# Kernel tuning notes

Measured on AMD Instinct MI355X. Metric: run time of the kernel, lower is better.

## Reference

```python
import jax, jax.numpy as jnp
import numpy as np

B, C, H, W = 2, 256, 64, 64
FEAT = 256          # in_channels * expansion_ratio
HEADS = 8
HS = FEAT // HEADS  # 32
OUT = 256


def setup_inputs() -> dict:
    key = jax.random.key(0)
    ks = jax.random.split(key, 12)
    inp = {
        "x": jax.random.normal(ks[0], (B, C, H, W), jnp.float32),
        "mod_multiplier": jax.random.normal(ks[1], (B, FEAT), jnp.float32),
        "mod_bias": jax.random.normal(ks[2], (B, FEAT), jnp.float32),
        # learned parameters (1x1 convs as matrices)
        "w_qkv": jax.random.normal(ks[3], (3 * FEAT, C), jnp.float32) * 0.02,
        "b_qkv": jnp.zeros((3 * FEAT,), jnp.float32),
        "w_proj": jax.random.normal(ks[4], (OUT, FEAT), jnp.float32) * 0.02,
        "pe_q_h": jax.random.normal(ks[5], (1, FEAT, H, 1), jnp.float32) * 0.02,
        "pe_q_w": jax.random.normal(ks[6], (1, FEAT, 1, W), jnp.float32) * 0.02,
        "pe_k_h": jax.random.normal(ks[7], (1, FEAT, H, 1), jnp.float32) * 0.02,
        "pe_k_w": jax.random.normal(ks[8], (1, FEAT, 1, W), jnp.float32) * 0.02,
        "pre_act_bias": jnp.zeros((1, C, 1, 1), jnp.float32),
        "pre_qkv_bias": jnp.zeros((1, C, 1, 1), jnp.float32),
        "pre_proj_bias": jnp.zeros((1, FEAT, 1, 1), jnp.float32),
        "id_scale": jnp.ones((1, OUT, 1, 1), jnp.float32),
    }
    return inp


def reference(x, mod_multiplier, mod_bias, w_qkv, b_qkv, w_proj,
              pe_q_h, pe_q_w, pe_k_h, pe_k_w,
              pre_act_bias, pre_qkv_bias, pre_proj_bias, id_scale):
    b = x.shape[0]
    # pre-activation (Fixup-style biases)
    x_preact = jax.nn.silu(x + pre_act_bias) + pre_qkv_bias
    # 1x1 conv -> QKV: [b, 3F, H, W]
    qkv = jnp.einsum('bchw,oc->bohw', x_preact, w_qkv) + b_qkv[None, :, None, None]
    q, k, v = jnp.split(qkv, 3, axis=1)
    # additive positional embeddings
    q = q + pe_q_h + pe_q_w
    k = k + pe_k_h + pe_k_w
    # FiLM modulation of query
    q = q * mod_multiplier[:, :, None, None] + mod_bias[:, :, None, None]
    # [b, heads, head_size, H*W]
    q = q.reshape(b, HEADS, HS, H * W)
    k = k.reshape(b, HEADS, HS, H * W)
    v = v.reshape(b, HEADS, HS, H * W)
    scale = jnp.asarray(HS ** 0.5, x.dtype)
    logits = jnp.einsum('bhdn,bhdm->bhnm', q, k) / scale
    weights = jax.nn.softmax(logits, axis=-1)
    attn = jnp.einsum('bhnm,bhdm->bhdn', weights, v)
    attn = attn.reshape(b, FEAT, H, W)
    # output projection (1x1 conv, no bias)
    x_res = jnp.einsum('bchw,oc->bohw', attn + pre_proj_bias, w_proj)
    return x * id_scale + x_res
```

## Files before the change

### kernel.cpp

```cpp
#include <hip/hip_runtime.h>
#include <hip/hip_bf16.h>
#include <cstdint>

#define NB   2
#define NC   256
#define NN   4096
#define NH   8
#define HSZ  32
#define NF   256
#define N3F  768

typedef __bf16 bf16x8 __attribute__((ext_vector_type(8)));
typedef __bf16 bf16x4 __attribute__((ext_vector_type(4)));
typedef short  s16x4  __attribute__((ext_vector_type(4)));
typedef float  floatx4 __attribute__((ext_vector_type(4)));

#define QSCALE 0.25506601622184f

__global__ void k_prep(const float* __restrict__ x, const float* __restrict__ pab,
                       const float* __restrict__ pqb, __bf16* __restrict__ y,
                       const float* __restrict__ wqkv, const float* __restrict__ wproj,
                       __bf16* __restrict__ wqb, __bf16* __restrict__ wpb) {
    __shared__ __bf16 ct[32 * 264];
    int bid = blockIdx.x, tid = threadIdx.x;
    if (bid >= 256) {
        int id = (bid - 256) * 1024 + tid * 4;
        const float* src = (id < 196608) ? (wqkv + id) : (wproj + (id - 196608));
        __bf16* dst = (id < 196608) ? (wqb + id) : (wpb + (id - 196608));
        float4 v = *(const float4*)src;
        bf16x4 o;
        o[0] = (__bf16)v.x; o[1] = (__bf16)v.y; o[2] = (__bf16)v.z; o[3] = (__bf16)v.w;
        *(bf16x4*)dst = o;
        return;
    }
    int b = bid >> 7, nt = bid & 127;
    int n0 = nt * 32;
    int cbase = tid >> 3, nc = tid & 7;
#pragma unroll
    for (int q = 0; q < 8; q++) {
        int c = cbase + q * 32;
        const float4 xv = *(const float4*)(x + ((size_t)b * NC + c) * NN + n0 + nc * 4);
        float bias = pab[c], qb = pqb[c];
        float vs[4] = {xv.x, xv.y, xv.z, xv.w};
#pragma unroll
        for (int i = 0; i < 4; i++) {
            float s = vs[i] + bias;
            float r = s / (1.f + __expf(-s)) + qb;
            ct[(nc * 4 + i) * 264 + c] = (__bf16)r;
        }
    }
    __syncthreads();
#pragma unroll
    for (int q = 0; q < 4; q++) {
        int id = tid + q * 256;
        int n = id >> 5, ck = (id & 31) * 8;
        bf16x8 v = *(const bf16x8*)(ct + n * 264 + ck);
        *(bf16x8*)(y + ((size_t)b * NN + n0 + n) * NC + ck) = v;
    }
}

__launch_bounds__(256)
__global__ void k_qkv(const __bf16* __restrict__ y, const __bf16* __restrict__ wb,
                      const float* __restrict__ bqkv,
                      const float* __restrict__ peqh, const float* __restrict__ peqw,
                      const float* __restrict__ pekh, const float* __restrict__ pekw,
                      const float* __restrict__ mm, const float* __restrict__ mb,
                      __bf16* __restrict__ qs, __bf16* __restrict__ kf, __bf16* __restrict__ vf) {
    __shared__ __bf16 smem[4][64 * 40];
    __bf16* ct = &smem[0][0];
    const int nt = blockIdx.x, ot = blockIdx.y, b = blockIdx.z;
    const int tid = threadIdx.x;
    const int wave = tid >> 6, lane = tid & 63, ln = lane & 15, quad = lane >> 4;
    const int wm = (wave & 1) * 32, wn = (wave >> 1) * 32;
    floatx4 acc[2][2];
#pragma unroll
    for (int i = 0; i < 2; i++)
#pragma unroll
        for (int j = 0; j < 2; j++) acc[i][j] = 0.f;
    const __bf16* ysrc = y + ((size_t)b * NN + nt * 64) * NC;
    const __bf16* wsrc = wb + (size_t)ot * 64 * NC;
    const int r0 = tid >> 2, c0 = (tid & 3) * 8;
    bf16x8 ya = *(const bf16x8*)(ysrc + (size_t)r0 * NC + c0);
    bf16x8 wa = *(const bf16x8*)(wsrc + (size_t)r0 * NC + c0);
    for (int ko = 0; ko < 8; ko++) {
        int buf = ko & 1;
        *(bf16x8*)(&smem[buf][r0 * 40 + c0]) = ya;
        *(bf16x8*)(&smem[2 + buf][r0 * 40 + c0]) = wa;
        __syncthreads();
        if (ko < 7) {
            int kc = (ko + 1) * 32;
            ya = *(const bf16x8*)(ysrc + (size_t)r0 * NC + kc + c0);
            wa = *(const bf16x8*)(wsrc + (size_t)r0 * NC + kc + c0);
        }
        bf16x8 af[2], bfr[2];
#pragma unroll
        for (int ii = 0; ii < 2; ii++) af[ii]  = *(const bf16x8*)(&smem[buf][(wm + ii * 16 + ln) * 40 + quad * 8]);
#pragma unroll
        for (int jj = 0; jj < 2; jj++) bfr[jj] = *(const bf16x8*)(&smem[2 + buf][(wn + jj * 16 + ln) * 40 + quad * 8]);
#pragma unroll
        for (int ii = 0; ii < 2; ii++)
#pragma unroll
            for (int jj = 0; jj < 2; jj++)
                acc[ii][jj] = __builtin_amdgcn_mfma_f32_16x16x32_bf16(af[ii], bfr[jj], acc[ii][jj], 0, 0, 0);
    }
    __syncthreads();
    if (ot < 8) {
#pragma unroll
        for (int ii = 0; ii < 2; ii++)
#pragma unroll
            for (int jj = 0; jj < 2; jj++) {
                int o_l = wn + jj * 16 + ln;
                int o_g = ot * 64 + o_l;
                float bq = bqkv[o_g];
#pragma unroll
                for (int r = 0; r < 4; r++) {
                    int n_l = wm + ii * 16 + quad * 4 + r;
                    float val = acc[ii][jj][r] + bq;
                    if (ot < 4) {
                        val += peqh[o_g * 64 + nt] + peqw[o_g * 64 + n_l];
                        val = val * mm[b * NF + o_g] + mb[b * NF + o_g];
                        val *= QSCALE;
                    } else {
                        int c = o_g - 256;
                        val += pekh[c * 64 + nt] + pekw[c * 64 + n_l];
                    }
                    ct[n_l * 72 + o_l] = (__bf16)val;
                }
            }
        __syncthreads();
#pragma unroll
        for (int q = 0; q < 2; q++) {
            int id = tid + q * 256;
            int n_l = id >> 3, oc = (id & 7) * 8;
            bf16x8 v = *(const bf16x8*)(ct + n_l * 72 + oc);
            int n_g = nt * 64 + n_l;
            int o_g = ot * 64 + oc;
            if (ot < 4) {
                int h = o_g >> 5, d = o_g & 31;
                *(bf16x8*)(qs + (((size_t)b * NH + h) * NN + n_g) * HSZ + d) = v;
            } else {
                int c = o_g - 256, h = c >> 5, d0 = c & 31;
                size_t blk = ((size_t)(b * NH + h) * 256 + (n_g >> 4)) * 512;
                *(bf16x8*)(kf + blk + (d0 >> 3) * 128 + (n_g & 15) * 8) = v;
            }
        }
    } else {
#pragma unroll
        for (int ii = 0; ii < 2; ii++)
#pragma unroll
            for (int jj = 0; jj < 2; jj++) {
                int o_l = wn + jj * 16 + ln;
                float bq = bqkv[ot * 64 + o_l];
#pragma unroll
                for (int r = 0; r < 4; r++) {
                    int n_l = wm + ii * 16 + quad * 4 + r;
                    ct[o_l * 72 + n_l] = (__bf16)(acc[ii][jj][r] + bq);
                }
            }
        __syncthreads();
#pragma unroll
        for (int q = 0; q < 4; q++) {
            int id = tid + q * 256;
            int o_l = id >> 4, ng4 = (id & 15) * 4;
            bf16x4 v = *(const bf16x4*)(ct + o_l * 72 + ng4);
            int c = (ot - 8) * 64 + o_l, h = c >> 5, d = c & 31;
            int dj = d >> 4, lnv = d & 15;
            int m_g = nt * 64 + ng4;
            size_t blk = ((size_t)(b * NH + h) * 256 + (m_g >> 4)) * 512;
            *(bf16x4*)(vf + blk + (((m_g >> 2) & 3) * 16 + lnv) * 8 + dj * 4) = v;
        }
    }
}

__launch_bounds__(256)
__global__ void k_attn(const __bf16* __restrict__ qs, const __bf16* __restrict__ kf,
                       const __bf16* __restrict__ vf,
                       __bf16* __restrict__ po, float* __restrict__ pl) {
    __shared__ __bf16 sbuf[2 * 8192];
    int bi = blockIdx.x;
    int xcd = bi & 7, r = bi >> 3;
    int bh = xcd * 2 + (r & 1);
    int r2 = r >> 1;
    int qt = r2 & 31, half = r2 >> 5;
    int tid = threadIdx.x, wave = tid >> 6, lane = tid & 63, ln = lane & 15, quad = lane >> 4;
    int n0 = qt * 128 + wave * 32;
    const __bf16* qbase = qs + (size_t)bh * NN * HSZ;
    const __bf16* kfb = kf + ((size_t)bh * 256 + half * 128) * 512;
    const __bf16* vfb = vf + ((size_t)bh * 256 + half * 128) * 512;
    bf16x8 qa[2];
    qa[0] = *(const bf16x8*)(qbase + (size_t)(n0 + ln) * HSZ + quad * 8);
    qa[1] = *(const bf16x8*)(qbase + (size_t)(n0 + 16 + ln) * HSZ + quad * 8);
    floatx4 o[2][2], o2[2];
    o[0][0] = 0.f; o[0][1] = 0.f; o[1][0] = 0.f; o[1][1] = 0.f;
    o2[0] = 0.f; o2[1] = 0.f;
    floatx4 zf = 0.f;
    s16x4 ones;
    ones[0] = (short)0x3F80; ones[1] = (short)0x3F80;
    ones[2] = (short)0x3F80; ones[3] = (short)0x3F80;
    const int toff = tid * 8;
    const int lo = lane * 8;
    bf16x8 kr0, kr1, vr0, vr1;
    kr0 = *(const bf16x8*)(kfb + toff);
    kr1 = *(const bf16x8*)(kfb + toff + 2048);
    vr0 = *(const bf16x8*)(vfb + toff);
    vr1 = *(const bf16x8*)(vfb + toff + 2048);
    for (int mt = 0; mt < 16; mt++) {
        int bo = (mt & 1) << 13;
        *(bf16x8*)(sbuf + bo + toff) = kr0;
        *(bf16x8*)(sbuf + bo + toff + 2048) = kr1;
        *(bf16x8*)(sbuf + bo + 4096 + toff) = vr0;
        *(bf16x8*)(sbuf + bo + 4096 + toff + 2048) = vr1;
        __syncthreads();
        if (mt < 15) {
            const __bf16* kn = kfb + (mt + 1) * 4096;
            const __bf16* vn = vfb + (mt + 1) * 4096;
            kr0 = *(const bf16x8*)(kn + toff);
            kr1 = *(const bf16x8*)(kn + toff + 2048);
            vr0 = *(const bf16x8*)(vn + toff);
            vr1 = *(const bf16x8*)(vn + toff + 2048);
        }
        const __bf16* kl = sbuf + bo;
        const __bf16* vl = sbuf + bo + 4096;
#pragma unroll
        for (int j = 0; j < 8; j++) {
            bf16x8 kfr = *(const bf16x8*)(kl + j * 512 + lo);
            bf16x8 vfr = *(const bf16x8*)(vl + j * 512 + lo);
            s16x4 vb0, vb1;
            __builtin_memcpy(&vb0, &vfr, 8);
            __builtin_memcpy(&vb1, (const char*)&vfr + 8, 8);
#pragma unroll
            for (int i = 0; i < 2; i++) {
                floatx4 s = __builtin_amdgcn_mfma_f32_16x16x32_bf16(kfr, qa[i], zf, 0, 0, 0);
                bf16x4 p;
#pragma unroll
                for (int rr = 0; rr < 4; rr++)
                    p[rr] = (__bf16)__builtin_amdgcn_exp2f(s[rr]);
                s16x4 pa;
                __builtin_memcpy(&pa, &p, 8);
                o[i][0] = __builtin_amdgcn_mfma_f32_16x16x16bf16_1k(pa, vb0, o[i][0], 0, 0, 0);
                o[i][1] = __builtin_amdgcn_mfma_f32_16x16x16bf16_1k(pa, vb1, o[i][1], 0, 0, 0);
                o2[i]   = __builtin_amdgcn_mfma_f32_16x16x16bf16_1k(pa, ones, o2[i], 0, 0, 0);
            }
        }
    }
    size_t plbase = (size_t)(half * 16 + bh) * NN;
    if (ln == 0)
#pragma unroll
        for (int i = 0; i < 2; i++)
#pragma unroll
            for (int rr = 0; rr < 4; rr++)
                pl[plbase + n0 + i * 16 + quad * 4 + rr] = o2[i][rr];
    __bf16* ct = sbuf;
#pragma unroll
    for (int i = 0; i < 2; i++)
#pragma unroll
        for (int dj = 0; dj < 2; dj++)
#pragma unroll
            for (int rr = 0; rr < 4; rr++)
                ct[(wave * 32 + i * 16 + quad * 4 + rr) * 32 + dj * 16 + ln] = (__bf16)o[i][dj][rr];
    __syncthreads();
    size_t pobase = ((size_t)(half * 16 + bh) * NN + (size_t)qt * 128) * HSZ;
#pragma unroll
    for (int q = 0; q < 2; q++) {
        int id = tid + q * 256;
        int n_l = id >> 2, dc = (id & 3) * 8;
        *(bf16x8*)(po + pobase + n_l * HSZ + dc) = *(const bf16x8*)(ct + n_l * 32 + dc);
    }
}

__launch_bounds__(256)
__global__ void k_proj(const __bf16* __restrict__ po, const float* __restrict__ pl,
                       const __bf16* __restrict__ wpb, const float* __restrict__ ppb,
                       const float* __restrict__ x, const float* __restrict__ idsc,
                       float* __restrict__ out) {
    __shared__ __bf16 at[64 * 264];
    __shared__ __bf16 bt[2][64 * 40];
    __shared__ float linv[8 * 64];
    __shared__ float ppbs[256];
    int nt = blockIdx.x, ot = blockIdx.y, b = blockIdx.z;
    int tid = threadIdx.x, wave = tid >> 6, lane = tid & 63, ln = lane & 15, quad = lane >> 4;
    int wo = (wave & 1) * 32, wn = (wave >> 1) * 32;
#pragma unroll
    for (int q = 0; q < 8; q++) {
        int id = tid + q * 256;
        int row = id >> 5, fc = (id & 31) * 8;
        *(bf16x8*)(at + row * 264 + fc) = *(const bf16x8*)(wpb + (size_t)(ot * 64 + row) * NF + fc);
    }
#pragma unroll
    for (int q = 0; q < 2; q++) {
        int id = tid + q * 256;
        int h = id >> 6, n_l = id & 63;
        size_t base = (size_t)(b * NH + h) * NN + nt * 64 + n_l;
        linv[id] = 1.f / (pl[base] + pl[base + (size_t)16 * NN]);
    }
    ppbs[tid] = ppb[tid];
    __syncthreads();
    floatx4 acc[2][2];
#pragma unroll
    for (int i = 0; i < 2; i++)
#pragma unroll
        for (int j = 0; j < 2; j++) acc[i][j] = 0.f;
    const int n_l = tid >> 2, dh8 = (tid & 3) * 8;
    const size_t hstep = (size_t)NN * HSZ;
    const size_t half_off = (size_t)16 * NN * HSZ;
    size_t prow = ((size_t)b * NH * NN + (size_t)nt * 64 + n_l) * HSZ + dh8;
    bf16x8 p0 = *(const bf16x8*)(po + prow);
    bf16x8 p1 = *(const bf16x8*)(po + prow + half_off);
    for (int ko = 0; ko < 8; ko++) {
        int buf = ko & 1;
        float iv = linv[ko * 64 + n_l];
        bf16x8 c;
#pragma unroll
        for (int e = 0; e < 8; e++)
            c[e] = (__bf16)(((float)p0[e] + (float)p1[e]) * iv + ppbs[ko * 32 + dh8 + e]);
        *(bf16x8*)(&bt[buf][n_l * 40 + dh8]) = c;
        __syncthreads();
        if (ko < 7) {
            size_t pr = prow + (size_t)(ko + 1) * hstep;
            p0 = *(const bf16x8*)(po + pr);
            p1 = *(const bf16x8*)(po + pr + half_off);
        }
        bf16x8 af[2], bfr[2];
#pragma unroll
        for (int oi = 0; oi < 2; oi++) af[oi]  = *(const bf16x8*)(at + (wo + oi * 16 + ln) * 264 + ko * 32 + quad * 8);
#pragma unroll
        for (int nj = 0; nj < 2; nj++) bfr[nj] = *(const bf16x8*)(&bt[buf][(wn + nj * 16 + ln) * 40 + quad * 8]);
#pragma unroll
        for (int oi = 0; oi < 2; oi++)
#pragma unroll
            for (int nj = 0; nj < 2; nj++)
                acc[oi][nj] = __builtin_amdgcn_mfma_f32_16x16x32_bf16(af[oi], bfr[nj], acc[oi][nj], 0, 0, 0);
    }
#pragma unroll
    for (int oi = 0; oi < 2; oi++)
#pragma unroll
        for (int nj = 0; nj < 2; nj++)
#pragma unroll
            for (int r = 0; r < 4; r++) {
                int o_g = ot * 64 + wo + oi * 16 + quad * 4 + r;
                int n_g = nt * 64 + wn + nj * 16 + ln;
                size_t idx = ((size_t)b * NF + o_g) * NN + n_g;
                out[idx] = x[idx] * idsc[o_g] + acc[oi][nj][r];
            }
}

extern "C" void kernel_launch(void* const* d_in, const int* in_sizes, int n_in,
                              void* d_out, int out_size, void* d_ws, size_t ws_size,
                              hipStream_t stream) {
    (void)in_sizes; (void)n_in; (void)out_size; (void)ws_size;
    const float* x    = (const float*)d_in[0];
    const float* mm   = (const float*)d_in[1];
    const float* mb   = (const float*)d_in[2];
    const float* wqkv = (const float*)d_in[3];
    const float* bqkv = (const float*)d_in[4];
    const float* wproj= (const float*)d_in[5];
    const float* peqh = (const float*)d_in[6];
    const float* peqw = (const float*)d_in[7];
    const float* pekh = (const float*)d_in[8];
    const float* pekw = (const float*)d_in[9];
    const float* pab  = (const float*)d_in[10];
    const float* pqb  = (const float*)d_in[11];
    const float* ppb  = (const float*)d_in[12];
    const float* idsc = (const float*)d_in[13];
    float* out = (float*)d_out;

    __bf16* ws = (__bf16*)d_ws;
    const size_t SEG = 2097152;
    __bf16* y    = ws;
    __bf16* qs   = ws + SEG;
    __bf16* kf   = ws + SEG * 2;
    __bf16* vf   = ws + SEG * 3;
    __bf16* po   = ws + SEG * 4;
    float*  pl   = (float*)(ws + SEG * 6);
    __bf16* wqb  = ws + SEG * 6 + 262144;
    __bf16* wpb  = wqb + 196608;

    hipLaunchKernelGGL(k_prep, dim3(512), dim3(256), 0, stream,
                       x, pab, pqb, y, wqkv, wproj, wqb, wpb);
    hipLaunchKernelGGL(k_qkv,  dim3(64, 12, 2), dim3(256), 0, stream,
                       y, wqb, bqkv, peqh, peqw, pekh, pekw, mm, mb, qs, kf, vf);
    hipLaunchKernelGGL(k_attn, dim3(1024), dim3(256), 0, stream, qs, kf, vf, po, pl);
    hipLaunchKernelGGL(k_proj, dim3(64, 4, 2), dim3(256), 0, stream,
                       po, pl, wpb, ppb, x, idsc, out);
}
```

Baseline: 177.8 us.

## Issue next-tile loads before barrier, raise MFMA priority, halve proj output tile

In the QKV, attention and projection loops, the global prefetch of the next K/V or input tile is now issued before the barrier. It goes into register double buffers, and the loops are unrolled by two so buffer indices stay static. The attention inner loop raises wave priority with s_setprio around the MFMA block. The projection kernel now computes 32 output channels per block instead of 64, doubling the grid for more parallelism. The cost is that each block redoes the normalisation and combination of the attention partials, and more registers are live.

```diff
diff --git a/kernel.cpp b/kernel.cpp
--- a/kernel.cpp
+++ b/kernel.cpp
@@ -80,23 +80,25 @@
     const __bf16* ysrc = y + ((size_t)b * NN + nt * 64) * NC;
     const __bf16* wsrc = wb + (size_t)ot * 64 * NC;
     const int r0 = tid >> 2, c0 = (tid & 3) * 8;
-    bf16x8 ya = *(const bf16x8*)(ysrc + (size_t)r0 * NC + c0);
-    bf16x8 wa = *(const bf16x8*)(wsrc + (size_t)r0 * NC + c0);
+    bf16x8 ya[2], wa[2];
+    ya[0] = *(const bf16x8*)(ysrc + (size_t)r0 * NC + c0);
+    wa[0] = *(const bf16x8*)(wsrc + (size_t)r0 * NC + c0);
+#pragma unroll 2
     for (int ko = 0; ko < 8; ko++) {
-        int buf = ko & 1;
-        *(bf16x8*)(&smem[buf][r0 * 40 + c0]) = ya;
-        *(bf16x8*)(&smem[2 + buf][r0 * 40 + c0]) = wa;
-        __syncthreads();
+        int cur = ko & 1, nxt = cur ^ 1;
+        *(bf16x8*)(&smem[cur][r0 * 40 + c0]) = ya[cur];
+        *(bf16x8*)(&smem[2 + cur][r0 * 40 + c0]) = wa[cur];
         if (ko < 7) {
             int kc = (ko + 1) * 32;
-            ya = *(const bf16x8*)(ysrc + (size_t)r0 * NC + kc + c0);
-            wa = *(const bf16x8*)(wsrc + (size_t)r0 * NC + kc + c0);
-        }
+            ya[nxt] = *(const bf16x8*)(ysrc + (size_t)r0 * NC + kc + c0);
+            wa[nxt] = *(const bf16x8*)(wsrc + (size_t)r0 * NC + kc + c0);
+        }
+        __syncthreads();
         bf16x8 af[2], bfr[2];
 #pragma unroll
-        for (int ii = 0; ii < 2; ii++) af[ii]  = *(const bf16x8*)(&smem[buf][(wm + ii * 16 + ln) * 40 + quad * 8]);
-#pragma unroll
-        for (int jj = 0; jj < 2; jj++) bfr[jj] = *(const bf16x8*)(&smem[2 + buf][(wn + jj * 16 + ln) * 40 + quad * 8]);
+        for (int ii = 0; ii < 2; ii++) af[ii]  = *(const bf16x8*)(&smem[cur][(wm + ii * 16 + ln) * 40 + quad * 8]);
+#pragma unroll
+        for (int jj = 0; jj < 2; jj++) bfr[jj] = *(const bf16x8*)(&smem[2 + cur][(wn + jj * 16 + ln) * 40 + quad * 8]);
 #pragma unroll
         for (int ii = 0; ii < 2; ii++)
 #pragma unroll
@@ -199,28 +201,31 @@
     ones[2] = (short)0x3F80; ones[3] = (short)0x3F80;
     const int toff = tid * 8;
     const int lo = lane * 8;
-    bf16x8 kr0, kr1, vr0, vr1;
-    kr0 = *(const bf16x8*)(kfb + toff);
-    kr1 = *(const bf16x8*)(kfb + toff + 2048);
-    vr0 = *(const bf16x8*)(vfb + toff);
-    vr1 = *(const bf16x8*)(vfb + toff + 2048);
+    bf16x8 kra[2], krb[2], vra[2], vrb[2];
+    kra[0] = *(const bf16x8*)(kfb + toff);
+    krb[0] = *(const bf16x8*)(kfb + toff + 2048);
+    vra[0] = *(const bf16x8*)(vfb + toff);
+    vrb[0] = *(const bf16x8*)(vfb + toff + 2048);
+#pragma unroll 2
     for (int mt = 0; mt < 16; mt++) {
-        int bo = (mt & 1) << 13;
-        *(bf16x8*)(sbuf + bo + toff) = kr0;
-        *(bf16x8*)(sbuf + bo + toff + 2048) = kr1;
-        *(bf16x8*)(sbuf + bo + 4096 + toff) = vr0;
-        *(bf16x8*)(sbuf + bo + 4096 + toff + 2048) = vr1;
-        __syncthreads();
+        int cur = mt & 1, nxt = cur ^ 1;
+        int bo = cur << 13;
+        *(bf16x8*)(sbuf + bo + toff) = kra[cur];
+        *(bf16x8*)(sbuf + bo + toff + 2048) = krb[cur];
+        *(bf16x8*)(sbuf + bo + 4096 + toff) = vra[cur];
+        *(bf16x8*)(sbuf + bo + 4096 + toff + 2048) = vrb[cur];
         if (mt < 15) {
             const __bf16* kn = kfb + (mt + 1) * 4096;
             const __bf16* vn = vfb + (mt + 1) * 4096;
-            kr0 = *(const bf16x8*)(kn + toff);
-            kr1 = *(const bf16x8*)(kn + toff + 2048);
-            vr0 = *(const bf16x8*)(vn + toff);
-            vr1 = *(const bf16x8*)(vn + toff + 2048);
-        }
+            kra[nxt] = *(const bf16x8*)(kn + toff);
+            krb[nxt] = *(const bf16x8*)(kn + toff + 2048);
+            vra[nxt] = *(const bf16x8*)(vn + toff);
+            vrb[nxt] = *(const bf16x8*)(vn + toff + 2048);
+        }
+        __syncthreads();
         const __bf16* kl = sbuf + bo;
         const __bf16* vl = sbuf + bo + 4096;
+        __builtin_amdgcn_s_setprio(1);
 #pragma unroll
         for (int j = 0; j < 8; j++) {
             bf16x8 kfr = *(const bf16x8*)(kl + j * 512 + lo);
@@ -242,6 +247,7 @@
                 o2[i]   = __builtin_amdgcn_mfma_f32_16x16x16bf16_1k(pa, ones, o2[i], 0, 0, 0);
             }
         }
+        __builtin_amdgcn_s_setprio(0);
     }
     size_t plbase = (size_t)(half * 16 + bh) * NN;
     if (ln == 0)
@@ -273,18 +279,18 @@
                        const __bf16* __restrict__ wpb, const float* __restrict__ ppb,
                        const float* __restrict__ x, const float* __restrict__ idsc,
                        float* __restrict__ out) {
-    __shared__ __bf16 at[64 * 264];
+    __shared__ __bf16 at[32 * 264];
     __shared__ __bf16 bt[2][64 * 40];
     __shared__ float linv[8 * 64];
     __shared__ float ppbs[256];
     int nt = blockIdx.x, ot = blockIdx.y, b = blockIdx.z;
     int tid = threadIdx.x, wave = tid >> 6, lane = tid & 63, ln = lane & 15, quad = lane >> 4;
-    int wo = (wave & 1) * 32, wn = (wave >> 1) * 32;
-#pragma unroll
-    for (int q = 0; q < 8; q++) {
+    int wo = (wave & 1) * 16, wn = (wave >> 1) * 32;
+#pragma unroll
+    for (int q = 0; q < 4; q++) {
         int id = tid + q * 256;
         int row = id >> 5, fc = (id & 31) * 8;
-        *(bf16x8*)(at + row * 264 + fc) = *(const bf16x8*)(wpb + (size_t)(ot * 64 + row) * NF + fc);
+        *(bf16x8*)(at + row * 264 + fc) = *(const bf16x8*)(wpb + (size_t)(ot * 32 + row) * NF + fc);
     }
 #pragma unroll
     for (int q = 0; q < 2; q++) {
@@ -295,53 +301,47 @@
     }
     ppbs[tid] = ppb[tid];
     __syncthreads();
-    floatx4 acc[2][2];
-#pragma unroll
-    for (int i = 0; i < 2; i++)
-#pragma unroll
-        for (int j = 0; j < 2; j++) acc[i][j] = 0.f;
+    floatx4 acc[2];
+    acc[0] = 0.f; acc[1] = 0.f;
     const int n_l = tid >> 2, dh8 = (tid & 3) * 8;
     const size_t hstep = (size_t)NN * HSZ;
     const size_t half_off = (size_t)16 * NN * HSZ;
     size_t prow = ((size_t)b * NH * NN + (size_t)nt * 64 + n_l) * HSZ + dh8;
-    bf16x8 p0 = *(const bf16x8*)(po + prow);
-    bf16x8 p1 = *(const bf16x8*)(po + prow + half_off);
+    bf16x8 p0[2], p1[2];
+    p0[0] = *(const bf16x8*)(po + prow);
+    p1[0] = *(const bf16x8*)(po + prow + half_off);
+#pragma unroll 2
     for (int ko = 0; ko < 8; ko++) {
-        int buf = ko & 1;
+        int cur = ko & 1, nxt = cur ^ 1;
         float iv = linv[ko * 64 + n_l];
         bf16x8 c;
 #pragma unroll
         for (int e = 0; e < 8; e++)
-            c[e] = (__bf16)(((float)p0[e] + (float)p1[e]) * iv + ppbs[ko * 32 + dh8 + e]);
-        *(bf16x8*)(&bt[buf][n_l * 40 + dh8]) = c;
-        __syncthreads();
+            c[e] = (__bf16)(((float)p0[cur][e] + (float)p1[cur][e]) * iv + ppbs[ko * 32 + dh8 + e]);
+        *(bf16x8*)(&bt[cur][n_l * 40 + dh8]) = c;
         if (ko < 7) {
             size_t pr = prow + (size_t)(ko + 1) * hstep;
-            p0 = *(const bf16x8*)(po + pr);
-            p1 = *(const bf16x8*)(po + pr + half_off);
-        }
-        bf16x8 af[2], bfr[2];
-#pragma unroll
-        for (int oi = 0; oi < 2; oi++) af[oi]  = *(const bf16x8*)(at + (wo + oi * 16 + ln) * 264 + ko * 32 + quad * 8);
-#pragma unroll
-        for (int nj = 0; nj < 2; nj++) bfr[nj] = *(const bf16x8*)(&bt[buf][(wn + nj * 16 + ln) * 40 + quad * 8]);
-#pragma unroll
-        for (int oi = 0; oi < 2; oi++)
-#pragma unroll
-            for (int nj = 0; nj < 2; nj++)
-                acc[oi][nj] = __builtin_amdgcn_mfma_f32_16x16x32_bf16(af[oi], bfr[nj], acc[oi][nj], 0, 0, 0);
-    }
-#pragma unroll
-    for (int oi = 0; oi < 2; oi++)
+            p0[nxt] = *(const bf16x8*)(po + pr);
+            p1[nxt] = *(const bf16x8*)(po + pr + half_off);
+        }
+        __syncthreads();
+        bf16x8 af, bfr[2];
+        af = *(const bf16x8*)(at + (wo + ln) * 264 + ko * 32 + quad * 8);
+#pragma unroll
+        for (int nj = 0; nj < 2; nj++) bfr[nj] = *(const bf16x8*)(&bt[cur][(wn + nj * 16 + ln) * 40 + quad * 8]);
 #pragma unroll
         for (int nj = 0; nj < 2; nj++)
-#pragma unroll
-            for (int r = 0; r < 4; r++) {
-                int o_g = ot * 64 + wo + oi * 16 + quad * 4 + r;
-                int n_g = nt * 64 + wn + nj * 16 + ln;
-                size_t idx = ((size_t)b * NF + o_g) * NN + n_g;
-                out[idx] = x[idx] * idsc[o_g] + acc[oi][nj][r];
-            }
+            acc[nj] = __builtin_amdgcn_mfma_f32_16x16x32_bf16(af, bfr[nj], acc[nj], 0, 0, 0);
+    }
+#pragma unroll
+    for (int nj = 0; nj < 2; nj++)
+#pragma unroll
+        for (int r = 0; r < 4; r++) {
+            int o_g = ot * 32 + wo + quad * 4 + r;
+            int n_g = nt * 64 + wn + nj * 16 + ln;
+            size_t idx = ((size_t)b * NF + o_g) * NN + n_g;
+            out[idx] = x[idx] * idsc[o_g] + acc[nj][r];
+        }
 }
 
 extern "C" void kernel_launch(void* const* d_in, const int* in_sizes, int n_in,
@@ -380,6 +380,6 @@
     hipLaunchKernelGGL(k_qkv,  dim3(64, 12, 2), dim3(256), 0, stream,
                        y, wqb, bqkv, peqh, peqw, pekh, pekw, mm, mb, qs, kf, vf);
     hipLaunchKernelGGL(k_attn, dim3(1024), dim3(256), 0, stream, qs, kf, vf, po, pl);
-    hipLaunchKernelGGL(k_proj, dim3(64, 4, 2), dim3(256), 0, stream,
+    hipLaunchKernelGGL(k_proj, dim3(64, 8, 2), dim3(256), 0, stream,
                        po, pl, wpb, ppb, x, idsc, out);
 }
```

Result: faster. 171.6 us (-3.5%).
